# Performance work log

Measured on AMD Instinct MI355X. Metric: run time of the kernel, lower is better.

The kernel has to match this reference:

```python
import jax, jax.numpy as jnp
import numpy as np

N = 16777216
BETA = 0.5  # SmoothL1Loss beta

def setup_inputs() -> dict:
    key = jax.random.key(0)
    k1, k2, k3 = jax.random.split(key, 3)
    outs = jax.random.normal(k1, (N,), dtype=jnp.float32)
    labels = jax.random.uniform(k2, (N,), dtype=jnp.float32)
    lens = jax.random.randint(k3, (N,), 1, 1000, dtype=jnp.int64)
    return {"outs": outs, "labels": labels, "lens": lens}

def reference(outs, labels, lens):
    d = outs - labels
    ad = jnp.abs(d)
    # per-element SmoothL1 (beta=0.5); single scalar reduces to 'mean' == value itself
    sl1 = jnp.where(ad < BETA, 0.5 * d * d / BETA, ad - 0.5 * BETA)
    # skip elements whose abs error is within 1/len boundary
    boundary = 1.0 / lens.astype(jnp.float32)
    mask = ad >= boundary
    total = jnp.sum(jnp.where(mask, sl1, 0.0))
    return total.reshape(1)
```

## Files before the change

### kernel.cpp

```cpp
#include <hip/hip_runtime.h>


#define N_TOTAL 16777216
#define NVEC    (N_TOTAL / 4)
#define BLOCK   256
#define GRID    2048
#define ITERS   (NVEC / (BLOCK * GRID))

typedef float f32x4 __attribute__((ext_vector_type(4)));
typedef int   i32x4 __attribute__((ext_vector_type(4)));

__device__ __forceinline__ float sl1_term(float o, float l, int len) {
    float d  = o - l;
    float ad = fabsf(d);
    float v  = (ad < 0.5f) ? (d * d) : (ad - 0.25f);
    float boundary = 1.0f / (float)len;
    return (ad >= boundary) ? v : 0.0f;
}

__device__ __forceinline__ float consume4(f32x4 o, f32x4 l, i32x4 n) {
    float s = 0.0f;
    s += sl1_term(o.x, l.x, n.x);
    s += sl1_term(o.y, l.y, n.y);
    s += sl1_term(o.z, l.z, n.z);
    s += sl1_term(o.w, l.w, n.w);
    return s;
}

__global__ __launch_bounds__(BLOCK, 8) void RegressionLoss_45440753992375_kernel(
        const float* __restrict__ outs,
        const float* __restrict__ labels,
        const int*   __restrict__ lens,
        float* __restrict__ out) {
    const f32x4* o4 = (const f32x4*)outs;
    const f32x4* l4 = (const f32x4*)labels;
    const i32x4* n4 = (const i32x4*)lens;

    const int base = blockIdx.x * (BLOCK * ITERS) + threadIdx.x;

    f32x4 oA = __builtin_nontemporal_load(o4 + base);
    f32x4 lA = __builtin_nontemporal_load(l4 + base);
    i32x4 nA = n4[base];

    f32x4 oB = __builtin_nontemporal_load(o4 + base + BLOCK);
    f32x4 lB = __builtin_nontemporal_load(l4 + base + BLOCK);
    i32x4 nB = n4[base + BLOCK];

    float acc = 0.0f;
    #pragma unroll
    for (int it = 0; it < ITERS - 2; ++it) {
        const int idx = base + (it + 2) * BLOCK;
        f32x4 oC = __builtin_nontemporal_load(o4 + idx);
        f32x4 lC = __builtin_nontemporal_load(l4 + idx);
        i32x4 nC = n4[idx];

        acc += consume4(oA, lA, nA);

        oA = oB; lA = lB; nA = nB;
        oB = oC; lB = lC; nB = nC;
    }
    acc += consume4(oA, lA, nA);
    acc += consume4(oB, lB, nB);

    #pragma unroll
    for (int off = 32; off > 0; off >>= 1)
        acc += __shfl_down(acc, off, 64);

    __shared__ float smem[BLOCK / 64];
    const int lane = threadIdx.x & 63;
    const int wid  = threadIdx.x >> 6;
    if (lane == 0) smem[wid] = acc;
    __syncthreads();
    if (threadIdx.x == 0) {
        float bsum = smem[0] + smem[1] + smem[2] + smem[3];
        atomicAdd(out, bsum);
    }
}

extern "C" void kernel_launch(void* const* d_in, const int* in_sizes, int n_in,
                              void* d_out, int out_size, void* d_ws, size_t ws_size,
                              hipStream_t stream) {
    const float* outs   = (const float*)d_in[0];
    const float* labels = (const float*)d_in[1];
    const int*   lens   = (const int*)d_in[2];
    float* out = (float*)d_out;

    hipMemsetAsync(out, 0, sizeof(float), stream);

    RegressionLoss_45440753992375_kernel<<<GRID, BLOCK, 0, stream>>>(outs, labels, lens, out);
}
```

Before: 186.8 us.

## Deepen register prefetch pipeline to eight stages with fewer, longer blocks

Shrinks the grid from 2048 to 512 blocks, so each thread walks 32 vector iterations instead of 8. It keeps eight iterations of loads in flight through a register ring buffer instead of two, and makes the lens loads nontemporal as well. The goal is more outstanding memory requests per wave to saturate HBM bandwidth with fewer resident waves. The cost is higher register pressure, with launch bounds relaxed to 2 blocks per SM, and fewer blocks, which may leave some CUs underfilled.

```diff
diff --git a/kernel.cpp b/kernel.cpp
--- a/kernel.cpp
+++ b/kernel.cpp
@@ -4,8 +4,9 @@
 #define N_TOTAL 16777216
 #define NVEC    (N_TOTAL / 4)
 #define BLOCK   256
-#define GRID    2048
+#define GRID    512
 #define ITERS   (NVEC / (BLOCK * GRID))
+#define DEPTH   8
 
 typedef float f32x4 __attribute__((ext_vector_type(4)));
 typedef int   i32x4 __attribute__((ext_vector_type(4)));
@@ -27,7 +28,7 @@
     return s;
 }
 
-__global__ __launch_bounds__(BLOCK, 8) void RegressionLoss_45440753992375_kernel(
+__global__ __launch_bounds__(BLOCK, 2) void RegressionLoss_45440753992375_kernel(
         const float* __restrict__ outs,
         const float* __restrict__ labels,
         const int*   __restrict__ lens,
@@ -38,29 +39,33 @@
 
     const int base = blockIdx.x * (BLOCK * ITERS) + threadIdx.x;
 
-    f32x4 oA = __builtin_nontemporal_load(o4 + base);
-    f32x4 lA = __builtin_nontemporal_load(l4 + base);
-    i32x4 nA = n4[base];
-
-    f32x4 oB = __builtin_nontemporal_load(o4 + base + BLOCK);
-    f32x4 lB = __builtin_nontemporal_load(l4 + base + BLOCK);
-    i32x4 nB = n4[base + BLOCK];
+    f32x4 o_s[DEPTH]; f32x4 l_s[DEPTH]; i32x4 n_s[DEPTH];
+    #pragma unroll
+    for (int j = 0; j < DEPTH; ++j) {
+        o_s[j] = __builtin_nontemporal_load(o4 + base + j * BLOCK);
+        l_s[j] = __builtin_nontemporal_load(l4 + base + j * BLOCK);
+        n_s[j] = __builtin_nontemporal_load(n4 + base + j * BLOCK);
+    }
 
     float acc = 0.0f;
     #pragma unroll
-    for (int it = 0; it < ITERS - 2; ++it) {
-        const int idx = base + (it + 2) * BLOCK;
-        f32x4 oC = __builtin_nontemporal_load(o4 + idx);
-        f32x4 lC = __builtin_nontemporal_load(l4 + idx);
-        i32x4 nC = n4[idx];
+    for (int it = 0; it < ITERS - DEPTH; ++it) {
+        const int idx = base + (it + DEPTH) * BLOCK;
+        f32x4 oN = __builtin_nontemporal_load(o4 + idx);
+        f32x4 lN = __builtin_nontemporal_load(l4 + idx);
+        i32x4 nN = __builtin_nontemporal_load(n4 + idx);
 
-        acc += consume4(oA, lA, nA);
+        acc += consume4(o_s[0], l_s[0], n_s[0]);
 
-        oA = oB; lA = lB; nA = nB;
-        oB = oC; lB = lC; nB = nC;
+        #pragma unroll
+        for (int j = 0; j < DEPTH - 1; ++j) {
+            o_s[j] = o_s[j + 1]; l_s[j] = l_s[j + 1]; n_s[j] = n_s[j + 1];
+        }
+        o_s[DEPTH - 1] = oN; l_s[DEPTH - 1] = lN; n_s[DEPTH - 1] = nN;
     }
-    acc += consume4(oA, lA, nA);
-    acc += consume4(oB, lB, nB);
+    #pragma unroll
+    for (int j = 0; j < DEPTH; ++j)
+        acc += consume4(o_s[j], l_s[j], n_s[j]);
 
     #pragma unroll
     for (int off = 32; off > 0; off >>= 1)
```

New measurement: 177.4 us. 5.1% less time.
